# Kernel tuning notes

Hardware: AMD Instinct MI355X
Metric: run time of the kernel (lower is better)

The kernel has to match this reference:

```python
import jax, jax.numpy as jnp
import numpy as np

N_NODES = 100000
N_EDGES = 1600000
D_IN = 128
D_HID = 128
LATENT = 64
N_GRAPHS = 512


def setup_inputs() -> dict:
    key = jax.random.key(0)
    ks = jax.random.split(key, 10)
    x = jax.random.normal(ks[0], (N_NODES, D_IN), dtype=jnp.float32)
    edge_index = jax.random.randint(ks[1], (2, N_EDGES), 0, N_NODES, dtype=jnp.int64)
    batch = jnp.sort(jax.random.randint(ks[2], (N_NODES,), 0, N_GRAPHS, dtype=jnp.int64))
    def lin(k, fan_in, fan_out):
        return jax.random.normal(k, (fan_in, fan_out), dtype=jnp.float32) / np.sqrt(fan_in)
    W1 = lin(ks[3], D_IN, D_HID); b1 = jnp.zeros((D_HID,), jnp.float32)
    W2 = lin(ks[4], D_HID, D_HID); b2 = jnp.zeros((D_HID,), jnp.float32)
    W3 = lin(ks[5], D_HID, 2 * LATENT); b3 = jnp.zeros((2 * LATENT,), jnp.float32)
    return {"x": x, "edge_index": edge_index, "batch": batch,
            "W1": W1, "b1": b1, "W2": W2, "b2": b2, "W3": W3, "b3": b3}


def _gcn_norm(edge_index, n_nodes):
    # PyG GCNConv default: add self-loops, symmetric normalization
    loop = jnp.arange(n_nodes, dtype=edge_index.dtype)
    src = jnp.concatenate([edge_index[0], loop])
    dst = jnp.concatenate([edge_index[1], loop])
    deg = jax.ops.segment_sum(jnp.ones_like(dst, dtype=jnp.float32), dst,
                              num_segments=n_nodes)
    dinv = jnp.where(deg > 0, jax.lax.rsqrt(deg), 0.0)
    norm = dinv[src] * dinv[dst]  # [E + N]
    return src, dst, norm


def _gcn_conv(x, W, b, src, dst, norm, n_nodes):
    h = x @ W                               # [N, d_out]
    msg = h[src] * norm[:, None]            # gather + scale, [E+N, d_out]
    agg = jax.ops.segment_sum(msg, dst, num_segments=n_nodes)
    return agg + b


def reference(x, edge_index, batch, W1, b1, W2, b2, W3, b3):
    n = x.shape[0]
    src, dst, norm = _gcn_norm(edge_index, n)
    h = jax.nn.relu(_gcn_conv(x, W1, b1, src, dst, norm, n))
    h = jax.nn.relu(_gcn_conv(h, W2, b2, src, dst, norm, n))
    h = _gcn_conv(h, W3, b3, src, dst, norm, n)
    # scatter_mean over batch ids -> [num_graphs, 2*latent]
    cnt = jax.ops.segment_sum(jnp.ones((n,), jnp.float32), batch,
                              num_segments=N_GRAPHS)
    summed = jax.ops.segment_sum(h, batch, num_segments=N_GRAPHS)
    return summed / jnp.maximum(cnt, 1.0)[:, None]
```

## Files before the change

kernel.cpp:

```cpp
#include <hip/hip_runtime.h>
#include <stdint.h>

typedef unsigned short u16;
typedef unsigned int   u32;

#define N_NODES  100000
#define N_EDGES  1600000
#define DFEAT    128
#define N_GRAPHS 512

#define NBKT   391
#define NBLK_E 782
#define LBUF   8192

typedef float f32x4 __attribute__((ext_vector_type(4)));
typedef short s16x8 __attribute__((ext_vector_type(8)));

__device__ __forceinline__ float bflo(u32 u) { return __uint_as_float(u << 16); }
__device__ __forceinline__ float bfhi(u32 u) { return __uint_as_float(u & 0xffff0000u); }
__device__ __forceinline__ u16 f2bf(float f) {
  u32 u = __float_as_uint(f);
  return (u16)((u + 0x7fffu + ((u >> 16) & 1u)) >> 16);
}
__device__ __forceinline__ u32 pack2(float f0, float f1) {
  return (u32)f2bf(f0) | ((u32)f2bf(f1) << 16);
}

__device__ __forceinline__ int ld_src(const int* ei, int m, int e) {
  return m ? ei[2 * e] : ei[e];
}
__device__ __forceinline__ int ld_dst(const int* ei, int m, int e) {
  return m ? ei[2 * (N_EDGES + e)] : ei[N_EDGES + e];
}

__global__ __launch_bounds__(256) void prep_k(const int* __restrict__ ei, int* __restrict__ flag,
                                              const float* __restrict__ W1, const float* __restrict__ W2,
                                              const float* __restrict__ W3, u16* __restrict__ T1,
                                              u16* __restrict__ T2, u16* __restrict__ T3) {
  int t = threadIdx.x;
  if (blockIdx.x == 0) {
    if (t < 64) {
      int v = ei[2 * t + 1];
      unsigned long long m = __ballot(v != 0);
      if (t == 0) *flag = (m == 0ull) ? 1 : 0;
    }
    return;
  }
  const float* W = (blockIdx.x == 1) ? W1 : (blockIdx.x == 2) ? W2 : W3;
  u16* T         = (blockIdx.x == 1) ? T1 : (blockIdx.x == 2) ? T2 : T3;
  for (int i = t; i < DFEAT * DFEAT; i += 256) {
    int n = i >> 7, k = i & 127;
    T[i] = f2bf(W[k * DFEAT + n]);
  }
}


__global__ __launch_bounds__(256) void histA_k(const int* __restrict__ ei,
                                               const int* __restrict__ flag,
                                               int* __restrict__ ghist) {
  __shared__ int hist[NBKT];
  int t = threadIdx.x, b = blockIdx.x;
  for (int i = t; i < NBKT; i += 256) hist[i] = 0;
  __syncthreads();
  int m = *flag;
  int e0 = b * 2048;
#pragma unroll
  for (int p = 0; p < 8; p++) {
    int e = e0 + p * 256 + t;
    if (e < N_EDGES) atomicAdd(&hist[ld_dst(ei, m, e) >> 8], 1);
  }
  __syncthreads();
  for (int i = t; i < NBKT; i += 256) ghist[b * NBKT + i] = hist[i];
}

__global__ __launch_bounds__(256) void scanB1_k(int* __restrict__ ghist,
                                                int* __restrict__ gtot) {
  __shared__ int a[1024];
  __shared__ int ts[256];
  int t = threadIdx.x, k = blockIdx.x;
  for (int i = t; i < 1024; i += 256) a[i] = (i < NBLK_E) ? ghist[i * NBKT + k] : 0;
  __syncthreads();
  int b4 = t * 4;
  int x0 = a[b4], x1 = a[b4 + 1], x2 = a[b4 + 2], x3 = a[b4 + 3];
  int tot = x0 + x1 + x2 + x3;
  ts[t] = tot;
  for (int off = 1; off < 256; off <<= 1) {
    __syncthreads(); int add = (t >= off) ? ts[t - off] : 0;
    __syncthreads(); ts[t] += add;
  }
  __syncthreads();
  int excl = ts[t] - tot;
  a[b4] = excl; a[b4 + 1] = excl + x0; a[b4 + 2] = excl + x0 + x1; a[b4 + 3] = excl + x0 + x1 + x2;
  __syncthreads();
  for (int i = t; i < NBLK_E; i += 256) ghist[i * NBKT + k] = a[i];
  if (t == 255) gtot[k] = ts[255];
}

__global__ __launch_bounds__(512) void scanB2_k(const int* __restrict__ gtot,
                                                int* __restrict__ bbase) {
  __shared__ int tmp[512];
  int t = threadIdx.x;
  int v = (t < NBKT) ? gtot[t] : 0;
  tmp[t] = v;
  for (int off = 1; off < 512; off <<= 1) {
    __syncthreads(); int add = (t >= off) ? tmp[t - off] : 0;
    __syncthreads(); tmp[t] += add;
  }
  __syncthreads();
  if (t < NBKT) bbase[t] = tmp[t] - v;
  if (t == 0) bbase[NBKT] = N_EDGES;
}

__global__ __launch_bounds__(256) void scatterC_k(const int* __restrict__ ei,
                                                  const int* __restrict__ flag,
                                                  const int* __restrict__ obase,
                                                  const int* __restrict__ bbase,
                                                  u32* __restrict__ colpk) {
  __shared__ int cur[NBKT];
  int t = threadIdx.x, b = blockIdx.x;
  for (int i = t; i < NBKT; i += 256) cur[i] = bbase[i] + obase[b * NBKT + i];
  __syncthreads();
  int m = *flag;
  int e0 = b * 2048;
#pragma unroll
  for (int p = 0; p < 8; p++) {
    int e = e0 + p * 256 + t;
    if (e < N_EDGES) {
      int d = ld_dst(ei, m, e);
      int s = ld_src(ei, m, e);
      int pos = atomicAdd(&cur[d >> 8], 1);
      colpk[pos] = (u32)s | ((u32)(d & 255) << 24);
    }
  }
}

__global__ __launch_bounds__(256) void fillD_k(const int* __restrict__ bbase,
                                               const u32* __restrict__ colpk,
                                               int* __restrict__ colarr,
                                               int* __restrict__ rowptr,
                                               float* __restrict__ dinv) {
  __shared__ int hist[256];
  __shared__ int cur[256];
  __shared__ int lbuf[LBUF];
  int t = threadIdx.x, b = blockIdx.x;
  int base = bbase[b], end = bbase[b + 1], cnt = end - base;
  hist[t] = 0;
  __syncthreads();
  for (int i = t; i < cnt; i += 256) atomicAdd(&hist[colpk[base + i] >> 24], 1);
  __syncthreads();
  int c = hist[t];
  cur[t] = c;
  for (int off = 1; off < 256; off <<= 1) {
    __syncthreads(); int add = (t >= off) ? cur[t - off] : 0;
    __syncthreads(); cur[t] += add;
  }
  __syncthreads();
  int excl = cur[t] - c;
  int node = b * 256 + t;
  if (node < N_NODES) {
    rowptr[node] = base + excl;
    dinv[node] = rsqrtf((float)(c + 1));
  }
  if (b == NBKT - 1 && t == 0) rowptr[N_NODES] = N_EDGES;
  __syncthreads();
  cur[t] = excl;
  __syncthreads();
  for (int i = t; i < cnt; i += 256) {
    u32 v = colpk[base + i];
    int slot = atomicAdd(&cur[v >> 24], 1);
    if (slot < LBUF) lbuf[slot] = (int)(v & 0x00FFFFFFu);
  }
  __syncthreads();
  for (int i = t; i < cnt; i += 256) colarr[base + i] = lbuf[i];
}

#define LP 136

__global__ __launch_bounds__(256, 1) void gemm_scale_k(const void* __restrict__ Xv,
                                                       int x_is_f32,
                                                       const u16* __restrict__ Wt,
                                                       const float* __restrict__ dinv,
                                                       u16* __restrict__ Y, int nrows) {
  __shared__ u16 sX[128 * LP];
  __shared__ u16 sW[128 * LP];
  int tid = threadIdx.x;
  int r0 = blockIdx.x * 128;

  for (int c = tid; c < 2048; c += 256) {
    int row = c >> 4, off = (c & 15) * 8;
    *(uint4*)(&sW[row * LP + off]) = *(const uint4*)(Wt + row * DFEAT + off);
  }
  if (x_is_f32) {
    const float* Xf = (const float*)Xv;
    for (int c = tid; c < 2048; c += 256) {
      int row = c >> 4, off = (c & 15) * 8;
      int grow = r0 + row;
      uint4 o = make_uint4(0, 0, 0, 0);
      if (grow < nrows) {
        const float* px = Xf + (size_t)grow * DFEAT + off;
        float4 v0 = *(const float4*)px;
        float4 v1 = *(const float4*)(px + 4);
        o.x = pack2(v0.x, v0.y); o.y = pack2(v0.z, v0.w);
        o.z = pack2(v1.x, v1.y); o.w = pack2(v1.z, v1.w);
      }
      *(uint4*)(&sX[row * LP + off]) = o;
    }
  } else {
    const u16* Xb = (const u16*)Xv;
    for (int c = tid; c < 2048; c += 256) {
      int row = c >> 4, off = (c & 15) * 8;
      int grow = r0 + row;
      uint4 v = make_uint4(0, 0, 0, 0);
      if (grow < nrows) v = *(const uint4*)(Xb + (size_t)grow * DFEAT + off);
      *(uint4*)(&sX[row * LP + off]) = v;
    }
  }
  __syncthreads();

  int wave = tid >> 6, lane = tid & 63;
  int q = lane >> 4, r = lane & 15;
  int wr0 = wave * 32;

  f32x4 acc[2][8];
#pragma unroll
  for (int m = 0; m < 2; m++)
#pragma unroll
    for (int i = 0; i < 8; i++) acc[m][i] = (f32x4){0.f, 0.f, 0.f, 0.f};

#pragma unroll
  for (int kk = 0; kk < 4; kk++) {
    int k0 = kk * 32;
    s16x8 a0 = *(const s16x8*)(&sX[(wr0 + r) * LP + k0 + q * 8]);
    s16x8 a1 = *(const s16x8*)(&sX[(wr0 + 16 + r) * LP + k0 + q * 8]);
#pragma unroll
    for (int nt = 0; nt < 8; nt++) {
      s16x8 b = *(const s16x8*)(&sW[(nt * 16 + r) * LP + k0 + q * 8]);
      acc[0][nt] = __builtin_amdgcn_mfma_f32_16x16x32_bf16(a0, b, acc[0][nt], 0, 0, 0);
      acc[1][nt] = __builtin_amdgcn_mfma_f32_16x16x32_bf16(a1, b, acc[1][nt], 0, 0, 0);
    }
  }

#pragma unroll
  for (int m = 0; m < 2; m++) {
#pragma unroll
    for (int i = 0; i < 4; i++) {
      int grow = r0 + wr0 + m * 16 + q * 4 + i;
      if (grow < nrows) {
        float dv = dinv[grow];
#pragma unroll
        for (int nt = 0; nt < 8; nt++) {
          Y[(size_t)grow * DFEAT + nt * 16 + r] = f2bf(acc[m][nt][i] * dv);
        }
      }
    }
  }
}

struct Acc8 {
  float a0, a1, a2, a3, a4, a5, a6, a7;
  __device__ __forceinline__ void add(uint4 v) {
    a0 += bflo(v.x); a1 += bfhi(v.x); a2 += bflo(v.y); a3 += bfhi(v.y);
    a4 += bflo(v.z); a5 += bfhi(v.z); a6 += bflo(v.w); a7 += bfhi(v.w);
  }
};

__global__ __launch_bounds__(256) void agg_k(const u32* __restrict__ HS,
                                             const float* __restrict__ dinv,
                                             const int* __restrict__ rowptr,
                                             const int* __restrict__ colidx,
                                             const float* __restrict__ bias,
                                             u32* __restrict__ OUT, int do_relu) {
  int t = threadIdx.x;
  int node = blockIdx.x * 16 + (t >> 4);
  int fp = t & 15;

  int s = rowptr[node], e = rowptr[node + 1];

  Acc8 A;
  uint4 v = *(const uint4*)(HS + (size_t)node * 64 + fp * 4);
  A.a0 = bflo(v.x); A.a1 = bfhi(v.x); A.a2 = bflo(v.y); A.a3 = bfhi(v.y);
  A.a4 = bflo(v.z); A.a5 = bfhi(v.z); A.a6 = bflo(v.w); A.a7 = bfhi(v.w);

  for (int w = s; w < e; w += 16) {
    int c = (w + fp < e) ? colidx[w + fp] : 0;
    int n = min(16, e - w);
    int j = 0;
    for (; j + 8 <= n; j += 8) {
      int i0 = __shfl(c, j, 16),     i1 = __shfl(c, j + 1, 16);
      int i2 = __shfl(c, j + 2, 16), i3 = __shfl(c, j + 3, 16);
      int i4 = __shfl(c, j + 4, 16), i5 = __shfl(c, j + 5, 16);
      int i6 = __shfl(c, j + 6, 16), i7 = __shfl(c, j + 7, 16);
      uint4 w0 = *(const uint4*)(HS + (size_t)i0 * 64 + fp * 4);
      uint4 w1 = *(const uint4*)(HS + (size_t)i1 * 64 + fp * 4);
      uint4 w2 = *(const uint4*)(HS + (size_t)i2 * 64 + fp * 4);
      uint4 w3 = *(const uint4*)(HS + (size_t)i3 * 64 + fp * 4);
      uint4 w4 = *(const uint4*)(HS + (size_t)i4 * 64 + fp * 4);
      uint4 w5 = *(const uint4*)(HS + (size_t)i5 * 64 + fp * 4);
      uint4 w6 = *(const uint4*)(HS + (size_t)i6 * 64 + fp * 4);
      uint4 w7 = *(const uint4*)(HS + (size_t)i7 * 64 + fp * 4);
      A.add(w0); A.add(w1); A.add(w2); A.add(w3);
      A.add(w4); A.add(w5); A.add(w6); A.add(w7);
    }
    for (; j + 4 <= n; j += 4) {
      int i0 = __shfl(c, j, 16),     i1 = __shfl(c, j + 1, 16);
      int i2 = __shfl(c, j + 2, 16), i3 = __shfl(c, j + 3, 16);
      uint4 w0 = *(const uint4*)(HS + (size_t)i0 * 64 + fp * 4);
      uint4 w1 = *(const uint4*)(HS + (size_t)i1 * 64 + fp * 4);
      uint4 w2 = *(const uint4*)(HS + (size_t)i2 * 64 + fp * 4);
      uint4 w3 = *(const uint4*)(HS + (size_t)i3 * 64 + fp * 4);
      A.add(w0); A.add(w1); A.add(w2); A.add(w3);
    }
    for (; j < n; j++) {
      int i0 = __shfl(c, j, 16);
      uint4 w0 = *(const uint4*)(HS + (size_t)i0 * 64 + fp * 4);
      A.add(w0);
    }
  }

  float dv = dinv[node];
  float4 b0 = *(const float4*)(bias + fp * 8);
  float4 b1 = *(const float4*)(bias + fp * 8 + 4);
  float r0 = A.a0 * dv + b0.x, r1 = A.a1 * dv + b0.y;
  float r2 = A.a2 * dv + b0.z, r3 = A.a3 * dv + b0.w;
  float r4 = A.a4 * dv + b1.x, r5 = A.a5 * dv + b1.y;
  float r6 = A.a6 * dv + b1.z, r7 = A.a7 * dv + b1.w;
  if (do_relu) {
    r0 = fmaxf(r0, 0.f); r1 = fmaxf(r1, 0.f); r2 = fmaxf(r2, 0.f); r3 = fmaxf(r3, 0.f);
    r4 = fmaxf(r4, 0.f); r5 = fmaxf(r5, 0.f); r6 = fmaxf(r6, 0.f); r7 = fmaxf(r7, 0.f);
  }
  uint4 o;
  o.x = pack2(r0, r1); o.y = pack2(r2, r3); o.z = pack2(r4, r5); o.w = pack2(r6, r7);
  *(uint4*)(OUT + (size_t)node * 64 + fp * 4) = o;
}

__device__ __forceinline__ int lower_bound_i(const int* a, int n, int key, int shift) {
  int lo = 0, hi = n;
  while (lo < hi) {
    int mid = (lo + hi) >> 1;
    if (a[mid << shift] < key) lo = mid + 1; else hi = mid;
  }
  return lo;
}

__global__ __launch_bounds__(256) void pool_k(const u32* __restrict__ H,
                                              const int* __restrict__ batch,
                                              const int* __restrict__ flag,
                                              float* __restrict__ OUT) {
  int g = blockIdx.x;
  int m = *flag;
  int lo = lower_bound_i(batch, N_NODES, g, m);
  int hi = lower_bound_i(batch, N_NODES, g + 1, m);
  int cnt = hi - lo;
  int d2 = threadIdx.x & 63;
  int half = threadIdx.x >> 6;
  float a0 = 0.f, a1 = 0.f;
  for (int row = lo + half; row < hi; row += 4) {
    u32 v = H[(size_t)row * 64 + d2];
    a0 += bflo(v); a1 += bfhi(v);
  }
  __shared__ float red0[256], red1[256];
  red0[threadIdx.x] = a0; red1[threadIdx.x] = a1;
  __syncthreads();
  if (threadIdx.x < 64) {
    float s0 = red0[d2] + red0[d2 + 64] + red0[d2 + 128] + red0[d2 + 192];
    float s1 = red1[d2] + red1[d2 + 64] + red1[d2 + 128] + red1[d2 + 192];
    float inv = 1.0f / fmaxf((float)cnt, 1.0f);
    OUT[g * DFEAT + 2 * d2]     = s0 * inv;
    OUT[g * DFEAT + 2 * d2 + 1] = s1 * inv;
  }
}


extern "C" void kernel_launch(void* const* d_in, const int* in_sizes, int n_in,
                              void* d_out, int out_size, void* d_ws, size_t ws_size,
                              hipStream_t stream) {
  const float* x   = (const float*)d_in[0];
  const int* ei    = (const int*)d_in[1];
  const int* batch = (const int*)d_in[2];
  const float* W1  = (const float*)d_in[3];
  const float* b1  = (const float*)d_in[4];
  const float* W2  = (const float*)d_in[5];
  const float* b2  = (const float*)d_in[6];
  const float* W3  = (const float*)d_in[7];
  const float* b3  = (const float*)d_in[8];
  float* out = (float*)d_out;

  char* p = (char*)d_ws;
  size_t off = 0;
  auto carve = [&](size_t bytes) -> void* {
    void* q = p + off;
    off = (off + bytes + 255) & ~(size_t)255;
    return q;
  };
  int*   flag   = (int*)carve(256);
  int*   ghist  = (int*)carve((size_t)NBLK_E * NBKT * 4);
  int*   gtot   = (int*)carve(NBKT * 4);
  int*   bbase  = (int*)carve((NBKT + 1) * 4);
  int*   rowptr = (int*)carve((N_NODES + 1) * 4);
  float* dinv   = (float*)carve(N_NODES * 4);
  u32*   colpk  = (u32*)carve((size_t)N_EDGES * 4);
  int*   colarr = (int*)carve((size_t)N_EDGES * 4);
  u16*   Wt1    = (u16*)carve(DFEAT * DFEAT * 2);
  u16*   Wt2    = (u16*)carve(DFEAT * DFEAT * 2);
  u16*   Wt3    = (u16*)carve(DFEAT * DFEAT * 2);
  u32*   bufA   = (u32*)carve((size_t)N_NODES * 64 * 4);
  u32*   bufB   = (u32*)carve((size_t)N_NODES * 64 * 4);
  (void)ws_size;

  prep_k<<<4, 256, 0, stream>>>(ei, flag, W1, W2, W3, Wt1, Wt2, Wt3);
  histA_k<<<NBLK_E, 256, 0, stream>>>(ei, flag, ghist);
  scanB1_k<<<NBKT, 256, 0, stream>>>(ghist, gtot);
  scanB2_k<<<1, 512, 0, stream>>>(gtot, bbase);
  scatterC_k<<<NBLK_E, 256, 0, stream>>>(ei, flag, ghist, bbase, colpk);
  fillD_k<<<NBKT, 256, 0, stream>>>(bbase, colpk, colarr, rowptr, dinv);

  const int GB = (N_NODES + 127) / 128;
  const int AB = N_NODES / 16;

  gemm_scale_k<<<GB, 256, 0, stream>>>((const void*)x, 1, Wt1, dinv, (u16*)bufA, N_NODES);
  agg_k<<<AB, 256, 0, stream>>>(bufA, dinv, rowptr, colarr, b1, bufB, 1);
  gemm_scale_k<<<GB, 256, 0, stream>>>((const void*)bufB, 0, Wt2, dinv, (u16*)bufA, N_NODES);
  agg_k<<<AB, 256, 0, stream>>>(bufA, dinv, rowptr, colarr, b2, bufB, 1);
  gemm_scale_k<<<GB, 256, 0, stream>>>((const void*)bufB, 0, Wt3, dinv, (u16*)bufA, N_NODES);
  agg_k<<<AB, 256, 0, stream>>>(bufA, dinv, rowptr, colarr, b3, bufB, 0);
  pool_k<<<N_GRAPHS, 256, 0, stream>>>(bufB, batch, flag, out);
}
```

Before: 412.9 us.

## Merge preprocessing kernels, enlarge edge chunks, and simplify aggregation index loads

```diff
diff --git a/kernel.cpp b/kernel.cpp
--- a/kernel.cpp
+++ b/kernel.cpp
@@ -10,7 +10,8 @@
 #define N_GRAPHS 512
 
 #define NBKT   391
-#define NBLK_E 782
+#define EPB    8192
+#define NBLK_E 196
 #define LBUF   8192
 
 typedef float f32x4 __attribute__((ext_vector_type(4)));
@@ -33,39 +34,51 @@
   return m ? ei[2 * (N_EDGES + e)] : ei[N_EDGES + e];
 }
 
-__global__ __launch_bounds__(256) void prep_k(const int* __restrict__ ei, int* __restrict__ flag,
-                                              const float* __restrict__ W1, const float* __restrict__ W2,
-                                              const float* __restrict__ W3, u16* __restrict__ T1,
-                                              u16* __restrict__ T2, u16* __restrict__ T3) {
+__device__ __forceinline__ int detect_m_block(const int* __restrict__ ei, int* sm) {
   int t = threadIdx.x;
-  if (blockIdx.x == 0) {
-    if (t < 64) {
-      int v = ei[2 * t + 1];
-      unsigned long long m = __ballot(v != 0);
-      if (t == 0) *flag = (m == 0ull) ? 1 : 0;
+  if (t < 64) {
+    int v = ei[2 * t + 1];
+    unsigned long long b = __ballot(v != 0);
+    if (t == 0) *sm = (b == 0ull) ? 1 : 0;
+  }
+  __syncthreads();
+  return *sm;
+}
+
+__global__ __launch_bounds__(256) void histA_k(const int* __restrict__ ei,
+                                               int* __restrict__ ghist,
+                                               const float* __restrict__ W1,
+                                               const float* __restrict__ W2,
+                                               const float* __restrict__ W3,
+                                               u16* __restrict__ T1, u16* __restrict__ T2,
+                                               u16* __restrict__ T3, int* __restrict__ flag) {
+  int t = threadIdx.x, b = blockIdx.x;
+  if (b >= NBLK_E) {
+    int r = b - NBLK_E;
+    if (r < 3) {
+      const float* W = (r == 0) ? W1 : (r == 1) ? W2 : W3;
+      u16* T         = (r == 0) ? T1 : (r == 1) ? T2 : T3;
+      for (int i = t; i < DFEAT * DFEAT; i += 256) {
+        int n = i >> 7, k = i & 127;
+        T[i] = f2bf(W[k * DFEAT + n]);
+      }
+    } else {
+      if (t < 64) {
+        int v = ei[2 * t + 1];
+        unsigned long long mm = __ballot(v != 0);
+        if (t == 0) *flag = (mm == 0ull) ? 1 : 0;
+      }
     }
     return;
   }
-  const float* W = (blockIdx.x == 1) ? W1 : (blockIdx.x == 2) ? W2 : W3;
-  u16* T         = (blockIdx.x == 1) ? T1 : (blockIdx.x == 2) ? T2 : T3;
-  for (int i = t; i < DFEAT * DFEAT; i += 256) {
-    int n = i >> 7, k = i & 127;
-    T[i] = f2bf(W[k * DFEAT + n]);
-  }
-}
-
-
-__global__ __launch_bounds__(256) void histA_k(const int* __restrict__ ei,
-                                               const int* __restrict__ flag,
-                                               int* __restrict__ ghist) {
+  __shared__ int sm;
   __shared__ int hist[NBKT];
-  int t = threadIdx.x, b = blockIdx.x;
+  int m = detect_m_block(ei, &sm);
   for (int i = t; i < NBKT; i += 256) hist[i] = 0;
   __syncthreads();
-  int m = *flag;
-  int e0 = b * 2048;
-#pragma unroll
-  for (int p = 0; p < 8; p++) {
+  int e0 = b * EPB;
+#pragma unroll
+  for (int p = 0; p < EPB / 256; p++) {
     int e = e0 + p * 256 + t;
     if (e < N_EDGES) atomicAdd(&hist[ld_dst(ei, m, e) >> 8], 1);
   }
@@ -75,55 +88,60 @@
 
 __global__ __launch_bounds__(256) void scanB1_k(int* __restrict__ ghist,
                                                 int* __restrict__ gtot) {
-  __shared__ int a[1024];
   __shared__ int ts[256];
   int t = threadIdx.x, k = blockIdx.x;
-  for (int i = t; i < 1024; i += 256) a[i] = (i < NBLK_E) ? ghist[i * NBKT + k] : 0;
-  __syncthreads();
-  int b4 = t * 4;
-  int x0 = a[b4], x1 = a[b4 + 1], x2 = a[b4 + 2], x3 = a[b4 + 3];
-  int tot = x0 + x1 + x2 + x3;
-  ts[t] = tot;
+  int v = (t < NBLK_E) ? ghist[t * NBKT + k] : 0;
+  ts[t] = v;
   for (int off = 1; off < 256; off <<= 1) {
     __syncthreads(); int add = (t >= off) ? ts[t - off] : 0;
     __syncthreads(); ts[t] += add;
   }
   __syncthreads();
-  int excl = ts[t] - tot;
-  a[b4] = excl; a[b4 + 1] = excl + x0; a[b4 + 2] = excl + x0 + x1; a[b4 + 3] = excl + x0 + x1 + x2;
-  __syncthreads();
-  for (int i = t; i < NBLK_E; i += 256) ghist[i * NBKT + k] = a[i];
+  if (t < NBLK_E) ghist[t * NBKT + k] = ts[t] - v;
   if (t == 255) gtot[k] = ts[255];
 }
 
-__global__ __launch_bounds__(512) void scanB2_k(const int* __restrict__ gtot,
-                                                int* __restrict__ bbase) {
-  __shared__ int tmp[512];
+__device__ __forceinline__ void scan_gtot_block(const int* __restrict__ gtot,
+                                                int* bb, int* sc) {
   int t = threadIdx.x;
-  int v = (t < NBKT) ? gtot[t] : 0;
-  tmp[t] = v;
-  for (int off = 1; off < 512; off <<= 1) {
-    __syncthreads(); int add = (t >= off) ? tmp[t - off] : 0;
-    __syncthreads(); tmp[t] += add;
-  }
-  __syncthreads();
-  if (t < NBKT) bbase[t] = tmp[t] - v;
-  if (t == 0) bbase[NBKT] = N_EDGES;
+  int v0 = gtot[t];
+  sc[t] = v0;
+  for (int off = 1; off < 256; off <<= 1) {
+    __syncthreads(); int add = (t >= off) ? sc[t - off] : 0;
+    __syncthreads(); sc[t] += add;
+  }
+  __syncthreads();
+  bb[t] = sc[t] - v0;
+  int base256 = sc[255];
+  __syncthreads();
+  int v1 = (t < NBKT - 256) ? gtot[256 + t] : 0;
+  sc[t] = v1;
+  for (int off = 1; off < 256; off <<= 1) {
+    __syncthreads(); int add = (t >= off) ? sc[t - off] : 0;
+    __syncthreads(); sc[t] += add;
+  }
+  __syncthreads();
+  if (t < NBKT - 256) bb[256 + t] = base256 + sc[t] - v1;
+  if (t == 0) bb[NBKT] = N_EDGES;
+  __syncthreads();
 }
 
 __global__ __launch_bounds__(256) void scatterC_k(const int* __restrict__ ei,
-                                                  const int* __restrict__ flag,
                                                   const int* __restrict__ obase,
-                                                  const int* __restrict__ bbase,
+                                                  const int* __restrict__ gtot,
                                                   u32* __restrict__ colpk) {
+  __shared__ int sm;
   __shared__ int cur[NBKT];
+  __shared__ int bb[NBKT + 1];
+  __shared__ int sc[256];
   int t = threadIdx.x, b = blockIdx.x;
-  for (int i = t; i < NBKT; i += 256) cur[i] = bbase[i] + obase[b * NBKT + i];
-  __syncthreads();
-  int m = *flag;
-  int e0 = b * 2048;
-#pragma unroll
-  for (int p = 0; p < 8; p++) {
+  int m = detect_m_block(ei, &sm);
+  scan_gtot_block(gtot, bb, sc);
+  for (int i = t; i < NBKT; i += 256) cur[i] = bb[i] + obase[b * NBKT + i];
+  __syncthreads();
+  int e0 = b * EPB;
+#pragma unroll
+  for (int p = 0; p < EPB / 256; p++) {
     int e = e0 + p * 256 + t;
     if (e < N_EDGES) {
       int d = ld_dst(ei, m, e);
@@ -134,7 +152,7 @@
   }
 }
 
-__global__ __launch_bounds__(256) void fillD_k(const int* __restrict__ bbase,
+__global__ __launch_bounds__(256) void fillD_k(const int* __restrict__ gtot,
                                                const u32* __restrict__ colpk,
                                                int* __restrict__ colarr,
                                                int* __restrict__ rowptr,
@@ -142,8 +160,11 @@
   __shared__ int hist[256];
   __shared__ int cur[256];
   __shared__ int lbuf[LBUF];
+  __shared__ int bb[NBKT + 1];
+  __shared__ int sc[256];
   int t = threadIdx.x, b = blockIdx.x;
-  int base = bbase[b], end = bbase[b + 1], cnt = end - base;
+  scan_gtot_block(gtot, bb, sc);
+  int base = bb[b], end = bb[b + 1], cnt = end - base;
   hist[t] = 0;
   __syncthreads();
   for (int i = t; i < cnt; i += 256) atomicAdd(&hist[colpk[base + i] >> 24], 1);
@@ -281,40 +302,19 @@
   A.a0 = bflo(v.x); A.a1 = bfhi(v.x); A.a2 = bflo(v.y); A.a3 = bfhi(v.y);
   A.a4 = bflo(v.z); A.a5 = bfhi(v.z); A.a6 = bflo(v.w); A.a7 = bfhi(v.w);
 
-  for (int w = s; w < e; w += 16) {
-    int c = (w + fp < e) ? colidx[w + fp] : 0;
-    int n = min(16, e - w);
-    int j = 0;
-    for (; j + 8 <= n; j += 8) {
-      int i0 = __shfl(c, j, 16),     i1 = __shfl(c, j + 1, 16);
-      int i2 = __shfl(c, j + 2, 16), i3 = __shfl(c, j + 3, 16);
-      int i4 = __shfl(c, j + 4, 16), i5 = __shfl(c, j + 5, 16);
-      int i6 = __shfl(c, j + 6, 16), i7 = __shfl(c, j + 7, 16);
-      uint4 w0 = *(const uint4*)(HS + (size_t)i0 * 64 + fp * 4);
-      uint4 w1 = *(const uint4*)(HS + (size_t)i1 * 64 + fp * 4);
-      uint4 w2 = *(const uint4*)(HS + (size_t)i2 * 64 + fp * 4);
-      uint4 w3 = *(const uint4*)(HS + (size_t)i3 * 64 + fp * 4);
-      uint4 w4 = *(const uint4*)(HS + (size_t)i4 * 64 + fp * 4);
-      uint4 w5 = *(const uint4*)(HS + (size_t)i5 * 64 + fp * 4);
-      uint4 w6 = *(const uint4*)(HS + (size_t)i6 * 64 + fp * 4);
-      uint4 w7 = *(const uint4*)(HS + (size_t)i7 * 64 + fp * 4);
-      A.add(w0); A.add(w1); A.add(w2); A.add(w3);
-      A.add(w4); A.add(w5); A.add(w6); A.add(w7);
-    }
-    for (; j + 4 <= n; j += 4) {
-      int i0 = __shfl(c, j, 16),     i1 = __shfl(c, j + 1, 16);
-      int i2 = __shfl(c, j + 2, 16), i3 = __shfl(c, j + 3, 16);
-      uint4 w0 = *(const uint4*)(HS + (size_t)i0 * 64 + fp * 4);
-      uint4 w1 = *(const uint4*)(HS + (size_t)i1 * 64 + fp * 4);
-      uint4 w2 = *(const uint4*)(HS + (size_t)i2 * 64 + fp * 4);
-      uint4 w3 = *(const uint4*)(HS + (size_t)i3 * 64 + fp * 4);
-      A.add(w0); A.add(w1); A.add(w2); A.add(w3);
-    }
-    for (; j < n; j++) {
-      int i0 = __shfl(c, j, 16);
-      uint4 w0 = *(const uint4*)(HS + (size_t)i0 * 64 + fp * 4);
-      A.add(w0);
-    }
+  int j = s;
+  for (; j + 4 <= e; j += 4) {
+    int i0 = colidx[j], i1 = colidx[j + 1], i2 = colidx[j + 2], i3 = colidx[j + 3];
+    uint4 w0 = *(const uint4*)(HS + (size_t)i0 * 64 + fp * 4);
+    uint4 w1 = *(const uint4*)(HS + (size_t)i1 * 64 + fp * 4);
+    uint4 w2 = *(const uint4*)(HS + (size_t)i2 * 64 + fp * 4);
+    uint4 w3 = *(const uint4*)(HS + (size_t)i3 * 64 + fp * 4);
+    A.add(w0); A.add(w1); A.add(w2); A.add(w3);
+  }
+  for (; j < e; j++) {
+    int i0 = colidx[j];
+    uint4 w0 = *(const uint4*)(HS + (size_t)i0 * 64 + fp * 4);
+    A.add(w0);
   }
 
   float dv = dinv[node];
@@ -395,7 +395,6 @@
   int*   flag   = (int*)carve(256);
   int*   ghist  = (int*)carve((size_t)NBLK_E * NBKT * 4);
   int*   gtot   = (int*)carve(NBKT * 4);
-  int*   bbase  = (int*)carve((NBKT + 1) * 4);
   int*   rowptr = (int*)carve((N_NODES + 1) * 4);
   float* dinv   = (float*)carve(N_NODES * 4);
   u32*   colpk  = (u32*)carve((size_t)N_EDGES * 4);
@@ -407,12 +406,10 @@
   u32*   bufB   = (u32*)carve((size_t)N_NODES * 64 * 4);
   (void)ws_size;
 
-  prep_k<<<4, 256, 0, stream>>>(ei, flag, W1, W2, W3, Wt1, Wt2, Wt3);
-  histA_k<<<NBLK_E, 256, 0, stream>>>(ei, flag, ghist);
+  histA_k<<<NBLK_E + 4, 256, 0, stream>>>(ei, ghist, W1, W2, W3, Wt1, Wt2, Wt3, flag);
   scanB1_k<<<NBKT, 256, 0, stream>>>(ghist, gtot);
-  scanB2_k<<<1, 512, 0, stream>>>(gtot, bbase);
-  scatterC_k<<<NBLK_E, 256, 0, stream>>>(ei, flag, ghist, bbase, colpk);
-  fillD_k<<<NBKT, 256, 0, stream>>>(bbase, colpk, colarr, rowptr, dinv);
+  scatterC_k<<<NBLK_E, 256, 0, stream>>>(ei, ghist, gtot, colpk);
+  fillD_k<<<NBKT, 256, 0, stream>>>(gtot, colpk, colarr, rowptr, dinv);
 
   const int GB = (N_NODES + 127) / 128;
   const int AB = N_NODES / 16;
```

Result: no change. 405.9 us (-1.7%).
